# Kernel optimization log

Hardware: AMD Instinct MI355X
Metric: run time of the kernel (lower is better)

Reference implementation:

```python
import jax, jax.numpy as jnp
import numpy as np

B, S, D, H = 2, 2048, 2048, 16
HD = D // H  # 128
L = 10  # adapter_len


def setup_inputs() -> dict:
    key = jax.random.key(0)
    ks = jax.random.split(key, 8)
    x = jax.random.normal(ks[0], (B, S, D), dtype=jnp.float32)
    wq = jax.random.normal(ks[1], (D, D), dtype=jnp.float32) * 0.02
    wk = jax.random.normal(ks[2], (D, D), dtype=jnp.float32) * 0.02
    wv = jax.random.normal(ks[3], (D, D), dtype=jnp.float32) * 0.02
    wo = jax.random.normal(ks[4], (D, D), dtype=jnp.float32) * 0.02
    adapter = jax.random.normal(ks[5], (1, L, D), dtype=jnp.float32)
    gate = jax.random.normal(ks[6], (1, H, 1, 1), dtype=jnp.float32) * 0.1
    # rotary frequencies (LLaMA style, theta=10000)
    inv_freq = 1.0 / (10000.0 ** (jnp.arange(0, HD, 2, dtype=jnp.float32) / HD))
    t = jnp.arange(S, dtype=jnp.float32)
    ang = jnp.outer(t, inv_freq)  # [S, HD//2]
    freqs_cos = jnp.cos(ang)
    freqs_sin = jnp.sin(ang)
    # additive causal mask [1,1,S,S]
    mask = jnp.triu(jnp.full((S, S), -1e9, dtype=jnp.float32), k=1)[None, None]
    return {"x": x, "wq": wq, "wk": wk, "wv": wv, "wo": wo,
            "adapter": adapter, "gate": gate,
            "freqs_cos": freqs_cos, "freqs_sin": freqs_sin, "mask": mask}


def _rope(v, cos, sin):
    # v: [B,S,H,HD]; cos/sin: [S, HD//2]; complex multiply on (even, odd) pairs
    v = v.reshape(*v.shape[:-1], HD // 2, 2)
    v0, v1 = v[..., 0], v[..., 1]
    c = cos[None, :, None, :]
    s = sin[None, :, None, :]
    out = jnp.stack([v0 * c - v1 * s, v0 * s + v1 * c], axis=-1)
    return out.reshape(*out.shape[:-2], HD)


def reference(x, wq, wk, wv, wo, adapter, gate, freqs_cos, freqs_sin, mask):
    scale = 1.0 / np.sqrt(HD)
    xq = (x @ wq).reshape(B, S, H, HD)
    xk = (x @ wk).reshape(B, S, H, HD)
    xv = (x @ wv).reshape(B, S, H, HD)
    xq = _rope(xq, freqs_cos, freqs_sin)
    xk = _rope(xk, freqs_cos, freqs_sin)
    # self-attention with additive causal mask
    scores = jnp.einsum('bqhd,bkhd->bhqk', xq, xk) * scale + mask
    probs = jax.nn.softmax(scores.astype(jnp.float32), axis=-1).astype(xq.dtype)
    out = jnp.einsum('bhqk,bkhd->bqhd', probs, xv)  # [B,S,H,HD]
    # gated adapter cross-attention (no rotary on adapter K/V)
    ak = (adapter[0] @ wk).reshape(L, H, HD)
    av = (adapter[0] @ wv).reshape(L, H, HD)
    a_scores = jnp.einsum('bqhd,khd->bhqk', xq, ak) * scale
    a_probs = gate * jax.nn.softmax(a_scores.astype(jnp.float32), axis=-1).astype(xq.dtype)
    out = out + jnp.einsum('bhqk,khd->bqhd', a_probs, av)
    return out.reshape(B, S, D) @ wo
```

## Files before the change

### kernel.cpp

```cpp
#include <hip/hip_runtime.h>


typedef unsigned short ushort_t;
typedef unsigned int uint32;
typedef __attribute__((ext_vector_type(8))) short bf16x8;
typedef __attribute__((ext_vector_type(4))) float f32x4;

__device__ __forceinline__ void async16(void* lds, const void* g) {
  __builtin_amdgcn_global_load_lds((const __attribute__((address_space(1))) void*)g,
                                   (__attribute__((address_space(3))) void*)lds,
                                   16, 0, 0);
}
__device__ __forceinline__ ushort_t f2bf(float f) {
  uint32 u = __float_as_uint(f);
  u += 0x7FFFu + ((u >> 16) & 1u);
  return (ushort_t)(u >> 16);
}
__device__ __forceinline__ float bf2f(ushort_t b) {
  return __uint_as_float(((uint32)b) << 16);
}
__device__ __forceinline__ float dpp_xor1(float v) {
  return __int_as_float(__builtin_amdgcn_update_dpp(
      0, __float_as_int(v), 0xB1, 0xf, 0xf, true));
}
#define DPP_MAX(t, ctrl) \
  t = fmaxf(t, __int_as_float(__builtin_amdgcn_update_dpp( \
      0, __float_as_int(t), (ctrl), 0xf, 0xf, true)))
#define DPP_ADD(t, ctrl) \
  t += __int_as_float(__builtin_amdgcn_update_dpp( \
      0, __float_as_int(t), (ctrl), 0xf, 0xf, true))
__device__ __forceinline__ float rowmax16(float t) {
  DPP_MAX(t, 0xB1);
  DPP_MAX(t, 0x4E);
  t = fmaxf(t, __int_as_float(__builtin_amdgcn_ds_swizzle(
      __float_as_int(t), 0x101F)));
  DPP_MAX(t, 0x128);
  return t;
}
__device__ __forceinline__ float rowsum16(float t) {
  DPP_ADD(t, 0xB1);
  DPP_ADD(t, 0x4E);
  t += __int_as_float(__builtin_amdgcn_ds_swizzle(__float_as_int(t), 0x101F));
  DPP_ADD(t, 0x128);
  return t;
}

__global__ __launch_bounds__(256) void cast_x_kernel(const float* __restrict__ x,
                                                     ushort_t* __restrict__ Xb) {
  size_t i = ((size_t)blockIdx.x * 256 + threadIdx.x) * 8;
  float4 a = *(const float4*)(x + i);
  float4 b = *(const float4*)(x + i + 4);
  uint4 o;
  o.x = (uint32)f2bf(a.x) | ((uint32)f2bf(a.y) << 16);
  o.y = (uint32)f2bf(a.z) | ((uint32)f2bf(a.w) << 16);
  o.z = (uint32)f2bf(b.x) | ((uint32)f2bf(b.y) << 16);
  o.w = (uint32)f2bf(b.z) | ((uint32)f2bf(b.w) << 16);
  *(uint4*)(Xb + i) = o;
}

__global__ __launch_bounds__(256) void rope_pack_kernel(
    const float* __restrict__ fc, const float* __restrict__ fs,
    float2* __restrict__ fcs) {
  int i = blockIdx.x * 256 + threadIdx.x;
  fcs[i] = make_float2(fc[i], fs[i]);
}

__global__ __launch_bounds__(256) void transpose_w_kernel(
    const float* __restrict__ w0, const float* __restrict__ w1,
    const float* __restrict__ w2, const float* __restrict__ w3,
    ushort_t* __restrict__ outBase) {
  const float* W = (blockIdx.z == 0) ? w0 : (blockIdx.z == 1) ? w1
                 : (blockIdx.z == 2) ? w2 : w3;
  ushort_t* Wt = outBase + (size_t)blockIdx.z * 4194304;
  __shared__ float L[64][65];
  int t = threadIdx.x, tc = t & 63, tr = t >> 6;
  int k0 = blockIdx.x * 64, n0 = blockIdx.y * 64;
  for (int i = 0; i < 16; ++i) {
    int r = i * 4 + tr;
    L[r][tc] = W[(size_t)(k0 + r) * 2048 + n0 + tc];
  }
  __syncthreads();
  int tr8 = t >> 5, tc2 = t & 31;
  for (int i = 0; i < 8; ++i) {
    int r = i * 8 + tr8;
    uint32 pk = (uint32)f2bf(L[2 * tc2][r]) | ((uint32)f2bf(L[2 * tc2 + 1][r]) << 16);
    *(uint32*)(Wt + (size_t)(n0 + r) * 2048 + k0 + 2 * tc2) = pk;
  }
}

__global__ __launch_bounds__(256) void adapter_kv_kernel(
    const float* __restrict__ adapter, const float* __restrict__ wk,
    const float* __restrict__ wv, float* __restrict__ ak, float* __restrict__ av) {
  const float* W = blockIdx.z ? wv : wk;
  float* out = blockIdx.z ? av : ak;
  __shared__ float As[10][128];
  int t = threadIdx.x;
  int k0 = blockIdx.y * 128;
  for (int i = t; i < 1280; i += 256)
    As[i >> 7][i & 127] = adapter[(size_t)(i >> 7) * 2048 + k0 + (i & 127)];
  __syncthreads();
  int n = blockIdx.x * 256 + t;
  float acc[10];
#pragma unroll
  for (int l = 0; l < 10; ++l) acc[l] = 0.f;
  for (int kk = 0; kk < 128; ++kk) {
    float wv_ = W[(size_t)(k0 + kk) * 2048 + n];
#pragma unroll
    for (int l = 0; l < 10; ++l) acc[l] += As[l][kk] * wv_;
  }
#pragma unroll
  for (int l = 0; l < 10; ++l) atomicAdd(&out[l * 2048 + n], acc[l]);
}

__global__ __launch_bounds__(256) void adapter_pack_kernel(
    const float* __restrict__ ak, const float* __restrict__ av,
    ushort_t* __restrict__ akb, ushort_t* __restrict__ avb) {
  int t = blockIdx.x * 256 + threadIdx.x;
  if (t < 32768) {
    int h = t >> 11, l = (t >> 7) & 15, d = t & 127;
    akb[t] = (l < 10) ? f2bf(ak[l * 2048 + h * 128 + d]) : (ushort_t)0;
  }
  int h = t >> 12, d = (t >> 5) & 127, l = t & 31;
  avb[t] = (l < 10) ? f2bf(av[l * 2048 + h * 128 + d]) : (ushort_t)0;
}

#define QK_BARX() asm volatile("s_barrier" ::: "memory")
#define QK_LGKM0() asm volatile("s_waitcnt lgkmcnt(0)" ::: "memory")

__device__ __forceinline__ void kloop_128x256(
    char* lds, const ushort_t* __restrict__ A, const ushort_t* __restrict__ Bt,
    size_t bm0, size_t bn0, f32x4 (&acc)[4][4]) {
  const int tid = (int)threadIdx.x;
  const int w = tid >> 6, lane = tid & 63, quad = lane >> 4, l15 = lane & 15;
  const int wr = (w >> 2) * 64, wc = (w & 3) * 64;
  const int nt = 32;
  char* const pA0 = lds;
  char* const pA1 = lds + 16384;
  char* const pB0 = lds + 32768;
  char* const pB1 = lds + 65536;

#define PAT(T) (((T) & 1) ? pA1 : pA0)
#define PBT(T) (((T) & 1) ? pB1 : pB0)
#define SEGL(OP, LDSB, GROW, T)                                                \
  do {                                                                         \
    int rr_ = w * 8 + (lane >> 3);                                             \
    int cl_ = (lane & 7) ^ (rr_ & 7);                                          \
    async16((LDSB) + w * 1024,                                                 \
            (OP) + ((GROW) + (size_t)rr_) * 2048 + (size_t)((T) * 64 + cl_ * 8)); \
  } while (0)
#define ST_A(T)                                                                \
  do { if ((T) < nt) { SEGL(A, PAT(T), bm0, (T));                              \
                       SEGL(A, PAT(T) + 8192, bm0 + 64, (T)); } } while (0)
#define ST_B0(T)                                                               \
  do { if ((T) < nt) SEGL(Bt, PBT(T), bn0, (T)); } while (0)
#define ST_B123(T)                                                             \
  do { if ((T) < nt) { SEGL(Bt, PBT(T) + 8192,  bn0 + 64,  (T));               \
                       SEGL(Bt, PBT(T) + 16384, bn0 + 128, (T));               \
                       SEGL(Bt, PBT(T) + 24576, bn0 + 192, (T)); } } while (0)

  ST_A(0); ST_B0(0); ST_B123(0); ST_B123(1);
  asm volatile("s_waitcnt vmcnt(3)" ::: "memory");
  QK_BARX();

#pragma unroll 2
  for (int t = 0; t < nt; ++t) {
    const char* pA = PAT(t);
    const char* pB = PBT(t);
    bf16x8 bfv[4][2];
#pragma unroll
    for (int j = 0; j < 4; ++j) {
      int brow = wc + j * 16 + l15;
#pragma unroll
      for (int ks = 0; ks < 2; ++ks)
        bfv[j][ks] = *(const bf16x8*)(pB + brow * 128 +
                                      (((ks * 4 + quad) ^ (brow & 7)) * 16));
    }
#pragma unroll
    for (int ph = 0; ph < 2; ++ph) {
      bf16x8 af[2][2];
#pragma unroll
      for (int ii = 0; ii < 2; ++ii) {
        int arow = wr + (ph * 2 + ii) * 16 + l15;
#pragma unroll
        for (int ks = 0; ks < 2; ++ks)
          af[ii][ks] = *(const bf16x8*)(pA + arow * 128 +
                                        (((ks * 4 + quad) ^ (arow & 7)) * 16));
      }
      if (ph == 0) { ST_A(t + 1); ST_B0(t + 1); }
      else         { ST_B123(t + 2); }
      QK_BARX();
      QK_LGKM0();
      __builtin_amdgcn_s_setprio(1);
#pragma unroll
      for (int ks = 0; ks < 2; ++ks)
#pragma unroll
        for (int ii = 0; ii < 2; ++ii)
#pragma unroll
          for (int j = 0; j < 4; ++j)
            acc[ph * 2 + ii][j] = __builtin_amdgcn_mfma_f32_16x16x32_bf16(
                af[ii][ks], bfv[j][ks], acc[ph * 2 + ii][j], 0, 0, 0);
      __builtin_amdgcn_s_setprio(0);
      if (ph == 1) {
        if (t == nt - 2) asm volatile("s_waitcnt vmcnt(0)" ::: "memory");
        else             asm volatile("s_waitcnt vmcnt(3)" ::: "memory");
      }
      QK_BARX();
    }
  }
#undef PAT
#undef PBT
#undef SEGL
#undef ST_A
#undef ST_B0
#undef ST_B123
}

__global__ __launch_bounds__(512, 2) void gemm_qkv128_kernel(
    const ushort_t* __restrict__ A, const ushort_t* __restrict__ Bt,
    ushort_t* __restrict__ outQ, ushort_t* __restrict__ outK,
    ushort_t* __restrict__ Vt, const float2* __restrict__ fcs) {
  __shared__ char lds[98304];
  const int tid = (int)threadIdx.x;
  const int w = tid >> 6, lane = tid & 63, quad = lane >> 4, l15 = lane & 15;
  const int wr = (w >> 2) * 64, wc = (w & 3) * 64;

  const int wg = ((int)blockIdx.x & 7) * 96 + ((int)blockIdx.x >> 3);
  const size_t bm0 = (size_t)(wg & 31) * 128;
  const size_t bn0 = (size_t)(wg >> 5) * 256;

  f32x4 acc[4][4];
  f32x4 z4 = {0.f, 0.f, 0.f, 0.f};
#pragma unroll
  for (int i = 0; i < 4; ++i)
#pragma unroll
    for (int j = 0; j < 4; ++j) acc[i][j] = z4;

  kloop_128x256(lds, A, Bt, bm0, bn0, acc);

  const int seg = (int)(bn0 >> 11);
  if (seg < 2) {
    ushort_t* ob = seg ? outK : outQ;
#pragma unroll
    for (int i = 0; i < 4; ++i)
#pragma unroll
      for (int r = 0; r < 4; ++r) {
        size_t m = bm0 + wr + i * 16 + quad * 4 + r;
        int s = (int)(m & 2047);
#pragma unroll
        for (int j = 0; j < 4; ++j) {
          size_t n = (bn0 + wc + j * 16 + l15) & 2047;
          float v = acc[i][j][r];
          float v2 = dpp_xor1(v);
          int fi = ((int)n & 127) >> 1;
          float2 cs = fcs[s * 64 + fi];
          v = (lane & 1) ? (v2 * cs.y + v * cs.x) : (v * cs.x - v2 * cs.y);
          ob[m * 2048 + n] = f2bf(v);
        }
      }
  } else {
    char* T = lds + w * 8192;
#pragma unroll
    for (int i = 0; i < 4; ++i)
#pragma unroll
      for (int j = 0; j < 4; ++j) {
        int nn = j * 16 + l15;
        int md0 = i * 8 + quad * 2;
        uint32 p01 = (uint32)f2bf(acc[i][j][0]) | ((uint32)f2bf(acc[i][j][1]) << 16);
        uint32 p23 = (uint32)f2bf(acc[i][j][2]) | ((uint32)f2bf(acc[i][j][3]) << 16);
        *(uint32*)(T + nn * 128 + ((md0 ^ (nn & 31)) * 4)) = p01;
        *(uint32*)(T + nn * 128 + (((md0 + 1) ^ (nn & 31)) * 4)) = p23;
      }
    const int b = (int)(bm0 >> 11);
    const int s0 = (int)(bm0 & 2047) + wr;
    const int n2 = (int)(bn0 & 2047) + wc;
#pragma unroll
    for (int it = 0; it < 32; ++it) {
      int row = it * 2 + (lane >> 5);
      int pp = lane & 31;
      uint32 dv = *(const uint32*)(T + row * 128 + pp * 4);
      int md = pp ^ (row & 31);
      int nloc = n2 + row;
      size_t bh = (size_t)b * 16 + (nloc >> 7);
      *(uint32*)(Vt + (bh * 128 + (size_t)(nloc & 127)) * 2048 + s0 + 2 * md) = dv;
    }
  }
}

__global__ __launch_bounds__(512, 2) void gemm_wo_kernel(
    const ushort_t* __restrict__ A, const ushort_t* __restrict__ Bt,
    float* __restrict__ out) {
  __shared__ char lds[98304];
  const int tid = (int)threadIdx.x;
  const int w = tid >> 6, lane = tid & 63, quad = lane >> 4, l15 = lane & 15;
  const int wr = (w >> 2) * 64, wc = (w & 3) * 64;

  const int wg = ((int)blockIdx.x & 7) * 32 + ((int)blockIdx.x >> 3);
  const size_t bm0 = (size_t)(wg & 31) * 128;
  const size_t bn0 = (size_t)(wg >> 5) * 256;

  f32x4 acc[4][4];
  f32x4 z4 = {0.f, 0.f, 0.f, 0.f};
#pragma unroll
  for (int i = 0; i < 4; ++i)
#pragma unroll
    for (int j = 0; j < 4; ++j) acc[i][j] = z4;

  kloop_128x256(lds, A, Bt, bm0, bn0, acc);

#pragma unroll
  for (int i = 0; i < 4; ++i)
#pragma unroll
    for (int r = 0; r < 4; ++r) {
      size_t m = bm0 + wr + i * 16 + quad * 4 + r;
#pragma unroll
      for (int j = 0; j < 4; ++j) {
        size_t n = bn0 + wc + j * 16 + l15;
        out[m * 2048 + n] = acc[i][j][r];
      }
    }
}

__global__ __launch_bounds__(256) void flash_kernel(
    const ushort_t* __restrict__ Qb, const ushort_t* __restrict__ Kb,
    const ushort_t* __restrict__ Vt, const ushort_t* __restrict__ akb,
    const ushort_t* __restrict__ avb, const float* __restrict__ gate,
    ushort_t* __restrict__ Ob) {
  __shared__ char ldsK[16384];
  __shared__ char ldsV[16384];
  __shared__ char ldsP[16384];
  const int tid = threadIdx.x;
  const int w = tid >> 6, lane = tid & 63, quad = lane >> 4, l15 = lane & 15;
  const int idx = blockIdx.x;
  const int p = idx >> 8, c = idx & 255;
  const int u = c >> 4, vv = c & 15;
  const int qt = p ? (15 - u) : u;
  const int hb = (p << 4) | vv;
  const int h = hb >> 1, b = hb & 1;
  const float scale = 0.08838834764831845f;

  bf16x8 ones;
#pragma unroll
  for (int j = 0; j < 8; ++j) ones[j] = (short)0x3F80;

  bf16x8 qf[2][4];
#pragma unroll
  for (int mt = 0; mt < 2; ++mt) {
    size_t qrow = (size_t)qt * 128 + w * 32 + mt * 16 + l15;
    const ushort_t* base = Qb + ((size_t)b * 2048 + qrow) * 2048 + h * 128 + quad * 8;
#pragma unroll
    for (int ds = 0; ds < 4; ++ds) qf[mt][ds] = *(const bf16x8*)(base + ds * 32);
  }

  f32x4 zero4 = {0.f, 0.f, 0.f, 0.f};
  f32x4 oacc[2][8];
  f32x4 osum[2];
  float mrow[2][4];
#pragma unroll
  for (int mt = 0; mt < 2; ++mt) {
#pragma unroll
    for (int n8 = 0; n8 < 8; ++n8) oacc[mt][n8] = zero4;
    osum[mt] = zero4;
#pragma unroll
    for (int r = 0; r < 4; ++r) mrow[mt][r] = -1e30f;
  }

  const int ktmax = 2 * qt + 1;
  for (int kt = 0; kt <= ktmax; ++kt) {
#pragma unroll
    for (int ii = 0; ii < 4; ++ii) {
      int r0 = w * 16 + ii * 4;
      int row = r0 + (lane >> 4);
      int cl = (lane & 15) ^ (row & 15);
      async16(ldsK + r0 * 256,
              Kb + ((size_t)b * 2048 + kt * 64 + row) * 2048 + h * 128 + cl * 8);
    }
#pragma unroll
    for (int ii = 0; ii < 4; ++ii) {
      int d0 = w * 32 + ii * 8;
      int dr = d0 + (lane >> 3);
      int cl = (lane & 7) ^ (dr & 7);
      async16(ldsV + d0 * 128,
              Vt + ((size_t)(b * 16 + h) * 128 + dr) * 2048 + kt * 64 + cl * 8);
    }
    __syncthreads();

    f32x4 sacc[2][4];
#pragma unroll
    for (int mt = 0; mt < 2; ++mt)
#pragma unroll
      for (int nt = 0; nt < 4; ++nt) sacc[mt][nt] = zero4;
#pragma unroll
    for (int ds = 0; ds < 4; ++ds) {
      bf16x8 kf[4];
      int ch = ds * 4 + quad;
#pragma unroll
      for (int nt = 0; nt < 4; ++nt) {
        int row = nt * 16 + l15;
        kf[nt] = *(const bf16x8*)(ldsK + row * 256 + ((ch ^ (row & 15)) * 16));
      }
#pragma unroll
      for (int mt = 0; mt < 2; ++mt)
#pragma unroll
        for (int nt = 0; nt < 4; ++nt)
          sacc[mt][nt] = __builtin_amdgcn_mfma_f32_16x16x32_bf16(qf[mt][ds], kf[nt], sacc[mt][nt], 0, 0, 0);
    }

    const bool domask = (kt >= 2 * qt);
#pragma unroll
    for (int mt = 0; mt < 2; ++mt) {
      float tmax[4] = {-1e30f, -1e30f, -1e30f, -1e30f};
      const int qbase = qt * 128 + w * 32 + mt * 16 + quad * 4;
#pragma unroll
      for (int nt = 0; nt < 4; ++nt) {
        int kg = kt * 64 + nt * 16 + l15;
#pragma unroll
        for (int r = 0; r < 4; ++r) {
          float s = sacc[mt][nt][r] * scale;
          if (domask && kg > qbase + r) s = -1e30f;
          sacc[mt][nt][r] = s;
          tmax[r] = fmaxf(tmax[r], s);
        }
      }
#pragma unroll
      for (int r = 0; r < 4; ++r) {
        float t = rowmax16(tmax[r]);
        float mnew = fmaxf(mrow[mt][r], t);
        float alpha = __expf(mrow[mt][r] - mnew);
        mrow[mt][r] = mnew;
        osum[mt][r] *= alpha;
#pragma unroll
        for (int n8 = 0; n8 < 8; ++n8) oacc[mt][n8][r] *= alpha;
        tmax[r] = mnew;
      }
#pragma unroll
      for (int nt = 0; nt < 4; ++nt) {
        int col = nt * 16 + l15;
#pragma unroll
        for (int r = 0; r < 4; ++r) {
          float pv = __expf(sacc[mt][nt][r] - tmax[r]);
          int prow = w * 32 + mt * 16 + quad * 4 + r;
          int addr = prow * 128 + (((col >> 3) ^ (prow & 7)) * 16) + (col & 7) * 2;
          *(ushort_t*)(ldsP + addr) = f2bf(pv);
        }
      }
    }

#pragma unroll
    for (int ks = 0; ks < 2; ++ks) {
      int ch = ks * 4 + quad;
      bf16x8 pf[2];
#pragma unroll
      for (int mt = 0; mt < 2; ++mt) {
        int prow = w * 32 + mt * 16 + l15;
        pf[mt] = *(const bf16x8*)(ldsP + prow * 128 + ((ch ^ (prow & 7)) * 16));
      }
#pragma unroll
      for (int mt = 0; mt < 2; ++mt)
        osum[mt] = __builtin_amdgcn_mfma_f32_16x16x32_bf16(pf[mt], ones, osum[mt], 0, 0, 0);
#pragma unroll
      for (int n8 = 0; n8 < 8; ++n8) {
        int dr = n8 * 16 + l15;
        bf16x8 vf = *(const bf16x8*)(ldsV + dr * 128 + ((ch ^ (dr & 7)) * 16));
#pragma unroll
        for (int mt = 0; mt < 2; ++mt)
          oacc[mt][n8] = __builtin_amdgcn_mfma_f32_16x16x32_bf16(pf[mt], vf, oacc[mt][n8], 0, 0, 0);
      }
    }
    __syncthreads();
  }

  const float g = gate[h];
  {
    int row = w * 32 + (lane >> 1);
    int koff = 16 + (lane & 1) * 8;
    *(uint4*)(ldsP + row * 80 + koff * 2) = make_uint4(0, 0, 0, 0);
  }
  f32x4 sa[2] = {zero4, zero4};
#pragma unroll
  for (int ds = 0; ds < 4; ++ds) {
    bf16x8 kfa = *(const bf16x8*)(akb + ((size_t)h * 16 + l15) * 128 + ds * 32 + quad * 8);
#pragma unroll
    for (int mt = 0; mt < 2; ++mt)
      sa[mt] = __builtin_amdgcn_mfma_f32_16x16x32_bf16(qf[mt][ds], kfa, sa[mt], 0, 0, 0);
  }
#pragma unroll
  for (int mt = 0; mt < 2; ++mt) {
#pragma unroll
    for (int r = 0; r < 4; ++r) {
      float s = sa[mt][r] * scale;
      if (l15 >= 10) s = -1e30f;
      float mx = rowmax16(s);
      float e = __expf(s - mx);
      float sum = rowsum16(e);
      float pv = g * e / sum;
      int row = w * 32 + mt * 16 + quad * 4 + r;
      *(ushort_t*)(ldsP + row * 80 + l15 * 2) = f2bf(pv);
    }
  }
  bf16x8 paf[2];
#pragma unroll
  for (int mt = 0; mt < 2; ++mt)
    paf[mt] = *(const bf16x8*)(ldsP + (w * 32 + mt * 16 + l15) * 80 + quad * 16);

#pragma unroll
  for (int mt = 0; mt < 2; ++mt) {
    float rl[4];
#pragma unroll
    for (int r = 0; r < 4; ++r) rl[r] = 1.f / osum[mt][r];
#pragma unroll
    for (int n8 = 0; n8 < 8; ++n8)
#pragma unroll
      for (int r = 0; r < 4; ++r) oacc[mt][n8][r] *= rl[r];
  }
#pragma unroll
  for (int n8 = 0; n8 < 8; ++n8) {
    bf16x8 avf = *(const bf16x8*)(avb + ((size_t)h * 128 + n8 * 16 + l15) * 32 + quad * 8);
#pragma unroll
    for (int mt = 0; mt < 2; ++mt)
      oacc[mt][n8] = __builtin_amdgcn_mfma_f32_16x16x32_bf16(paf[mt], avf, oacc[mt][n8], 0, 0, 0);
  }
#pragma unroll
  for (int mt = 0; mt < 2; ++mt) {
    size_t qb0 = (size_t)qt * 128 + w * 32 + mt * 16 + quad * 4;
#pragma unroll
    for (int n8 = 0; n8 < 8; ++n8) {
      size_t col = (size_t)h * 128 + n8 * 16 + l15;
#pragma unroll
      for (int r = 0; r < 4; ++r)
        Ob[((size_t)b * 2048 + qb0 + r) * 2048 + col] = f2bf(oacc[mt][n8][r]);
    }
  }
}

extern "C" void kernel_launch(void* const* d_in, const int* in_sizes, int n_in,
                              void* d_out, int out_size, void* d_ws, size_t ws_size,
                              hipStream_t stream) {
  (void)in_sizes; (void)n_in; (void)out_size; (void)ws_size;
  const float* x       = (const float*)d_in[0];
  const float* wq      = (const float*)d_in[1];
  const float* wk      = (const float*)d_in[2];
  const float* wv      = (const float*)d_in[3];
  const float* wo      = (const float*)d_in[4];
  const float* adapter = (const float*)d_in[5];
  const float* gate    = (const float*)d_in[6];
  const float* fc      = (const float*)d_in[7];
  const float* fs      = (const float*)d_in[8];

  char* ws = (char*)d_ws;
  ushort_t* Xb   = (ushort_t*)(ws + 0);
  ushort_t* WtQ  = (ushort_t*)(ws + 16777216);
  ushort_t* WtO  = (ushort_t*)(ws + 41943040);
  ushort_t* Qb   = (ushort_t*)(ws + 50331648);
  ushort_t* Kb   = (ushort_t*)(ws + 67108864);
  ushort_t* Vt   = (ushort_t*)(ws + 83886080);
  float*    ak   = (float*)   (ws + 100663296);
  float*    av   = (float*)   (ws + 100745216);
  ushort_t* akb  = (ushort_t*)(ws + 100827136);
  ushort_t* avb  = (ushort_t*)(ws + 100892672);
  float2*   fcs  = (float2*)  (ws + 101023744);
  ushort_t* Ob   = Xb;

  cast_x_kernel<<<4096, 256, 0, stream>>>(x, Xb);
  rope_pack_kernel<<<512, 256, 0, stream>>>(fc, fs, fcs);
  transpose_w_kernel<<<dim3(32, 32, 4), 256, 0, stream>>>(wq, wk, wv, wo, WtQ);
  hipMemsetAsync(ak, 0, 163840, stream);
  adapter_kv_kernel<<<dim3(8, 16, 2), 256, 0, stream>>>(adapter, wk, wv, ak, av);
  adapter_pack_kernel<<<256, 256, 0, stream>>>(ak, av, akb, avb);
  gemm_qkv128_kernel<<<dim3(768), 512, 0, stream>>>(Xb, WtQ, Qb, Kb, Vt, fcs);
  flash_kernel<<<512, 256, 0, stream>>>(Qb, Kb, Vt, akb, avb, gate, Ob);
  gemm_wo_kernel<<<dim3(256), 512, 0, stream>>>(Ob, WtO, (float*)d_out);
}
```

Baseline: 444.9 us.

## Shrink flash attention Q tile to 64 rows and double grid size

The flash kernel now handles 64 query rows per block (16 per wave) instead of 128, doubling the grid to 1024 blocks with a new causal-balanced block ordering. It also skips the online-softmax rescale unless the running max grows by more than a threshold, packs P to bf16 pairs with a DPP swap plus a packed convert, and halves the P LDS buffer while requesting 4 blocks per CU. The aim is better occupancy and load balance on the causal triangle and less softmax overhead, at the cost of K/V tiles being reloaded by twice as many blocks.

```diff
diff --git a/kernel.cpp b/kernel.cpp
--- a/kernel.cpp
+++ b/kernel.cpp
@@ -320,21 +320,22 @@
     }
 }
 
-__global__ __launch_bounds__(256) void flash_kernel(
+__global__ __launch_bounds__(256, 4) void flash_kernel(
     const ushort_t* __restrict__ Qb, const ushort_t* __restrict__ Kb,
     const ushort_t* __restrict__ Vt, const ushort_t* __restrict__ akb,
     const ushort_t* __restrict__ avb, const float* __restrict__ gate,
     ushort_t* __restrict__ Ob) {
   __shared__ char ldsK[16384];
   __shared__ char ldsV[16384];
-  __shared__ char ldsP[16384];
+  __shared__ char ldsP[8192];
   const int tid = threadIdx.x;
   const int w = tid >> 6, lane = tid & 63, quad = lane >> 4, l15 = lane & 15;
   const int idx = blockIdx.x;
-  const int p = idx >> 8, c = idx & 255;
-  const int u = c >> 4, vv = c & 15;
-  const int qt = p ? (15 - u) : u;
-  const int hb = (p << 4) | vv;
+  const int pg = idx >> 8, c = idx & 255;
+  const int u = c >> 3, vv = c & 7;
+  const int uu = (pg & 2) ? ((u + 16) & 31) : u;
+  const int qt2 = (pg & 1) ? (31 - uu) : uu;
+  const int hb = (pg << 3) | vv;
   const int h = hb >> 1, b = hb & 1;
   const float scale = 0.08838834764831845f;
 
@@ -342,30 +343,24 @@
 #pragma unroll
   for (int j = 0; j < 8; ++j) ones[j] = (short)0x3F80;
 
-  bf16x8 qf[2][4];
-#pragma unroll
-  for (int mt = 0; mt < 2; ++mt) {
-    size_t qrow = (size_t)qt * 128 + w * 32 + mt * 16 + l15;
+  bf16x8 qf[4];
+  {
+    size_t qrow = (size_t)qt2 * 64 + w * 16 + l15;
     const ushort_t* base = Qb + ((size_t)b * 2048 + qrow) * 2048 + h * 128 + quad * 8;
 #pragma unroll
-    for (int ds = 0; ds < 4; ++ds) qf[mt][ds] = *(const bf16x8*)(base + ds * 32);
+    for (int ds = 0; ds < 4; ++ds) qf[ds] = *(const bf16x8*)(base + ds * 32);
   }
 
   f32x4 zero4 = {0.f, 0.f, 0.f, 0.f};
-  f32x4 oacc[2][8];
-  f32x4 osum[2];
-  float mrow[2][4];
-#pragma unroll
-  for (int mt = 0; mt < 2; ++mt) {
-#pragma unroll
-    for (int n8 = 0; n8 < 8; ++n8) oacc[mt][n8] = zero4;
-    osum[mt] = zero4;
-#pragma unroll
-    for (int r = 0; r < 4; ++r) mrow[mt][r] = -1e30f;
-  }
-
-  const int ktmax = 2 * qt + 1;
-  for (int kt = 0; kt <= ktmax; ++kt) {
+  f32x4 oacc[8];
+  f32x4 osum = zero4;
+  float mrow[4];
+#pragma unroll
+  for (int n8 = 0; n8 < 8; ++n8) oacc[n8] = zero4;
+#pragma unroll
+  for (int r = 0; r < 4; ++r) mrow[r] = -1e30f;
+
+  for (int kt = 0; kt <= qt2; ++kt) {
 #pragma unroll
     for (int ii = 0; ii < 4; ++ii) {
       int r0 = w * 16 + ii * 4;
@@ -384,11 +379,9 @@
     }
     __syncthreads();
 
-    f32x4 sacc[2][4];
-#pragma unroll
-    for (int mt = 0; mt < 2; ++mt)
-#pragma unroll
-      for (int nt = 0; nt < 4; ++nt) sacc[mt][nt] = zero4;
+    f32x4 sacc[4];
+#pragma unroll
+    for (int nt = 0; nt < 4; ++nt) sacc[nt] = zero4;
 #pragma unroll
     for (int ds = 0; ds < 4; ++ds) {
       bf16x8 kf[4];
@@ -399,71 +392,77 @@
         kf[nt] = *(const bf16x8*)(ldsK + row * 256 + ((ch ^ (row & 15)) * 16));
       }
 #pragma unroll
-      for (int mt = 0; mt < 2; ++mt)
-#pragma unroll
-        for (int nt = 0; nt < 4; ++nt)
-          sacc[mt][nt] = __builtin_amdgcn_mfma_f32_16x16x32_bf16(qf[mt][ds], kf[nt], sacc[mt][nt], 0, 0, 0);
-    }
-
-    const bool domask = (kt >= 2 * qt);
-#pragma unroll
-    for (int mt = 0; mt < 2; ++mt) {
-      float tmax[4] = {-1e30f, -1e30f, -1e30f, -1e30f};
-      const int qbase = qt * 128 + w * 32 + mt * 16 + quad * 4;
-#pragma unroll
-      for (int nt = 0; nt < 4; ++nt) {
-        int kg = kt * 64 + nt * 16 + l15;
+      for (int nt = 0; nt < 4; ++nt)
+        sacc[nt] = __builtin_amdgcn_mfma_f32_16x16x32_bf16(qf[ds], kf[nt], sacc[nt], 0, 0, 0);
+    }
+
+    const bool domask = (kt == qt2);
+    float tmax[4] = {-1e30f, -1e30f, -1e30f, -1e30f};
+    const int qbr = qt2 * 64 + w * 16 + quad * 4;
+#pragma unroll
+    for (int nt = 0; nt < 4; ++nt) {
+      int kg = kt * 64 + nt * 16 + l15;
+#pragma unroll
+      for (int r = 0; r < 4; ++r) {
+        float s = sacc[nt][r] * scale;
+        if (domask && kg > qbr + r) s = -1e30f;
+        sacc[nt][r] = s;
+        tmax[r] = fmaxf(tmax[r], s);
+      }
+    }
+    float need = 0.f;
+#pragma unroll
+    for (int r = 0; r < 4; ++r) {
+      tmax[r] = rowmax16(tmax[r]);
+      need = fmaxf(need, tmax[r] - mrow[r]);
+    }
+    if (__any(need > 8.0f)) {
+      float alpha[4];
+#pragma unroll
+      for (int r = 0; r < 4; ++r) {
+        float mnew = fmaxf(mrow[r], tmax[r]);
+        alpha[r] = __expf(mrow[r] - mnew);
+        osum[r] *= alpha[r];
+        mrow[r] = mnew;
+      }
+#pragma unroll
+      for (int n8 = 0; n8 < 8; ++n8)
+#pragma unroll
+        for (int r = 0; r < 4; ++r) oacc[n8][r] *= alpha[r];
+    }
+    uint32 pk[4][4];
+#pragma unroll
+    for (int nt = 0; nt < 4; ++nt)
+#pragma unroll
+      for (int r = 0; r < 4; ++r) {
+        float pv = __expf(sacc[nt][r] - mrow[r]);
+        float pn = dpp_xor1(pv);
+        uint32 d_;
+        asm volatile("v_cvt_pk_bf16_f32 %0, %1, %2" : "=v"(d_) : "v"(pv), "v"(pn));
+        pk[nt][r] = d_;
+      }
+    if (!(lane & 1)) {
+#pragma unroll
+      for (int nt = 0; nt < 4; ++nt)
 #pragma unroll
         for (int r = 0; r < 4; ++r) {
-          float s = sacc[mt][nt][r] * scale;
-          if (domask && kg > qbase + r) s = -1e30f;
-          sacc[mt][nt][r] = s;
-          tmax[r] = fmaxf(tmax[r], s);
+          int col = nt * 16 + l15;
+          int prow = w * 16 + quad * 4 + r;
+          *(uint32*)(ldsP + prow * 128 + (((col >> 3) ^ (prow & 7)) * 16) + (col & 7) * 2) = pk[nt][r];
         }
-      }
-#pragma unroll
-      for (int r = 0; r < 4; ++r) {
-        float t = rowmax16(tmax[r]);
-        float mnew = fmaxf(mrow[mt][r], t);
-        float alpha = __expf(mrow[mt][r] - mnew);
-        mrow[mt][r] = mnew;
-        osum[mt][r] *= alpha;
-#pragma unroll
-        for (int n8 = 0; n8 < 8; ++n8) oacc[mt][n8][r] *= alpha;
-        tmax[r] = mnew;
-      }
-#pragma unroll
-      for (int nt = 0; nt < 4; ++nt) {
-        int col = nt * 16 + l15;
-#pragma unroll
-        for (int r = 0; r < 4; ++r) {
-          float pv = __expf(sacc[mt][nt][r] - tmax[r]);
-          int prow = w * 32 + mt * 16 + quad * 4 + r;
-          int addr = prow * 128 + (((col >> 3) ^ (prow & 7)) * 16) + (col & 7) * 2;
-          *(ushort_t*)(ldsP + addr) = f2bf(pv);
-        }
-      }
     }
 
 #pragma unroll
     for (int ks = 0; ks < 2; ++ks) {
       int ch = ks * 4 + quad;
-      bf16x8 pf[2];
-#pragma unroll
-      for (int mt = 0; mt < 2; ++mt) {
-        int prow = w * 32 + mt * 16 + l15;
-        pf[mt] = *(const bf16x8*)(ldsP + prow * 128 + ((ch ^ (prow & 7)) * 16));
-      }
-#pragma unroll
-      for (int mt = 0; mt < 2; ++mt)
-        osum[mt] = __builtin_amdgcn_mfma_f32_16x16x32_bf16(pf[mt], ones, osum[mt], 0, 0, 0);
+      int prow = w * 16 + l15;
+      bf16x8 pf = *(const bf16x8*)(ldsP + prow * 128 + ((ch ^ (prow & 7)) * 16));
+      osum = __builtin_amdgcn_mfma_f32_16x16x32_bf16(pf, ones, osum, 0, 0, 0);
 #pragma unroll
       for (int n8 = 0; n8 < 8; ++n8) {
         int dr = n8 * 16 + l15;
         bf16x8 vf = *(const bf16x8*)(ldsV + dr * 128 + ((ch ^ (dr & 7)) * 16));
-#pragma unroll
-        for (int mt = 0; mt < 2; ++mt)
-          oacc[mt][n8] = __builtin_amdgcn_mfma_f32_16x16x32_bf16(pf[mt], vf, oacc[mt][n8], 0, 0, 0);
+        oacc[n8] = __builtin_amdgcn_mfma_f32_16x16x32_bf16(pf, vf, oacc[n8], 0, 0, 0);
       }
     }
     __syncthreads();
@@ -471,64 +470,47 @@
 
   const float g = gate[h];
   {
-    int row = w * 32 + (lane >> 1);
-    int koff = 16 + (lane & 1) * 8;
-    *(uint4*)(ldsP + row * 80 + koff * 2) = make_uint4(0, 0, 0, 0);
-  }
-  f32x4 sa[2] = {zero4, zero4};
+    int row = w * 16 + (lane >> 2);
+    *(uint2*)(ldsP + row * 80 + 32 + (lane & 3) * 8) = make_uint2(0, 0);
+  }
+  f32x4 sa = zero4;
 #pragma unroll
   for (int ds = 0; ds < 4; ++ds) {
     bf16x8 kfa = *(const bf16x8*)(akb + ((size_t)h * 16 + l15) * 128 + ds * 32 + quad * 8);
-#pragma unroll
-    for (int mt = 0; mt < 2; ++mt)
-      sa[mt] = __builtin_amdgcn_mfma_f32_16x16x32_bf16(qf[mt][ds], kfa, sa[mt], 0, 0, 0);
-  }
-#pragma unroll
-  for (int mt = 0; mt < 2; ++mt) {
-#pragma unroll
-    for (int r = 0; r < 4; ++r) {
-      float s = sa[mt][r] * scale;
-      if (l15 >= 10) s = -1e30f;
-      float mx = rowmax16(s);
-      float e = __expf(s - mx);
-      float sum = rowsum16(e);
-      float pv = g * e / sum;
-      int row = w * 32 + mt * 16 + quad * 4 + r;
-      *(ushort_t*)(ldsP + row * 80 + l15 * 2) = f2bf(pv);
-    }
-  }
-  bf16x8 paf[2];
-#pragma unroll
-  for (int mt = 0; mt < 2; ++mt)
-    paf[mt] = *(const bf16x8*)(ldsP + (w * 32 + mt * 16 + l15) * 80 + quad * 16);
-
-#pragma unroll
-  for (int mt = 0; mt < 2; ++mt) {
-    float rl[4];
-#pragma unroll
-    for (int r = 0; r < 4; ++r) rl[r] = 1.f / osum[mt][r];
-#pragma unroll
-    for (int n8 = 0; n8 < 8; ++n8)
-#pragma unroll
-      for (int r = 0; r < 4; ++r) oacc[mt][n8][r] *= rl[r];
-  }
+    sa = __builtin_amdgcn_mfma_f32_16x16x32_bf16(qf[ds], kfa, sa, 0, 0, 0);
+  }
+#pragma unroll
+  for (int r = 0; r < 4; ++r) {
+    float s = sa[r] * scale;
+    if (l15 >= 10) s = -1e30f;
+    float mx = rowmax16(s);
+    float e = __expf(s - mx);
+    float sum = rowsum16(e);
+    float pv = g * e / sum;
+    int row = w * 16 + quad * 4 + r;
+    *(ushort_t*)(ldsP + row * 80 + l15 * 2) = f2bf(pv);
+  }
+  bf16x8 paf = *(const bf16x8*)(ldsP + (w * 16 + l15) * 80 + quad * 16);
+
+  float rl[4];
+#pragma unroll
+  for (int r = 0; r < 4; ++r) rl[r] = 1.f / osum[r];
+#pragma unroll
+  for (int n8 = 0; n8 < 8; ++n8)
+#pragma unroll
+    for (int r = 0; r < 4; ++r) oacc[n8][r] *= rl[r];
 #pragma unroll
   for (int n8 = 0; n8 < 8; ++n8) {
     bf16x8 avf = *(const bf16x8*)(avb + ((size_t)h * 128 + n8 * 16 + l15) * 32 + quad * 8);
-#pragma unroll
-    for (int mt = 0; mt < 2; ++mt)
-      oacc[mt][n8] = __builtin_amdgcn_mfma_f32_16x16x32_bf16(paf[mt], avf, oacc[mt][n8], 0, 0, 0);
-  }
-#pragma unroll
-  for (int mt = 0; mt < 2; ++mt) {
-    size_t qb0 = (size_t)qt * 128 + w * 32 + mt * 16 + quad * 4;
-#pragma unroll
-    for (int n8 = 0; n8 < 8; ++n8) {
-      size_t col = (size_t)h * 128 + n8 * 16 + l15;
-#pragma unroll
-      for (int r = 0; r < 4; ++r)
-        Ob[((size_t)b * 2048 + qb0 + r) * 2048 + col] = f2bf(oacc[mt][n8][r]);
-    }
+    oacc[n8] = __builtin_amdgcn_mfma_f32_16x16x32_bf16(paf, avf, oacc[n8], 0, 0, 0);
+  }
+  size_t qb0 = (size_t)qt2 * 64 + w * 16 + quad * 4;
+#pragma unroll
+  for (int n8 = 0; n8 < 8; ++n8) {
+    size_t col = (size_t)h * 128 + n8 * 16 + l15;
+#pragma unroll
+    for (int r = 0; r < 4; ++r)
+      Ob[((size_t)b * 2048 + qb0 + r) * 2048 + col] = f2bf(oacc[n8][r]);
   }
 }
 
@@ -567,6 +549,6 @@
   adapter_kv_kernel<<<dim3(8, 16, 2), 256, 0, stream>>>(adapter, wk, wv, ak, av);
   adapter_pack_kernel<<<256, 256, 0, stream>>>(ak, av, akb, avb);
   gemm_qkv128_kernel<<<dim3(768), 512, 0, stream>>>(Xb, WtQ, Qb, Kb, Vt, fcs);
-  flash_kernel<<<512, 256, 0, stream>>>(Qb, Kb, Vt, akb, avb, gate, Ob);
+  flash_kernel<<<dim3(1024), 256, 0, stream>>>(Qb, Kb, Vt, akb, avb, gate, Ob);
   gemm_wo_kernel<<<dim3(256), 512, 0, stream>>>(Ob, WtO, (float*)d_out);
 }
```

After: 432.6 us. 1.03x faster.

## Add lazy softmax rescaling, packed bf16 P stores, and drop rope pack kernel

Applied to the files above, without the earlier changes.

In the flash kernel the online-softmax rescale of the output accumulators is now skipped unless some row's max has grown by more than a threshold, so the stale max is kept as the exponent reference. P values are converted in pairs with v_cvt_pk_bf16_f32 and written as 32-bit LDS stores from even lanes, which halves the number of stores. The separate rope_pack kernel is removed and the QKV GEMM epilogue reads cos and sin directly from the two tables. The costs are two gathered loads per element in the GEMM epilogue and a bounded exponent growth in P, which increases bf16 rounding risk.

```diff
diff --git a/kernel.cpp b/kernel.cpp
--- a/kernel.cpp
+++ b/kernel.cpp
@@ -56,13 +56,6 @@
   o.z = (uint32)f2bf(b.x) | ((uint32)f2bf(b.y) << 16);
   o.w = (uint32)f2bf(b.z) | ((uint32)f2bf(b.w) << 16);
   *(uint4*)(Xb + i) = o;
-}
-
-__global__ __launch_bounds__(256) void rope_pack_kernel(
-    const float* __restrict__ fc, const float* __restrict__ fs,
-    float2* __restrict__ fcs) {
-  int i = blockIdx.x * 256 + threadIdx.x;
-  fcs[i] = make_float2(fc[i], fs[i]);
 }
 
 __global__ __launch_bounds__(256) void transpose_w_kernel(
@@ -218,7 +211,8 @@
 __global__ __launch_bounds__(512, 2) void gemm_qkv128_kernel(
     const ushort_t* __restrict__ A, const ushort_t* __restrict__ Bt,
     ushort_t* __restrict__ outQ, ushort_t* __restrict__ outK,
-    ushort_t* __restrict__ Vt, const float2* __restrict__ fcs) {
+    ushort_t* __restrict__ Vt,
+    const float* __restrict__ fc, const float* __restrict__ fs) {
   __shared__ char lds[98304];
   const int tid = (int)threadIdx.x;
   const int w = tid >> 6, lane = tid & 63, quad = lane >> 4, l15 = lane & 15;
@@ -252,8 +246,9 @@
           float v = acc[i][j][r];
           float v2 = dpp_xor1(v);
           int fi = ((int)n & 127) >> 1;
-          float2 cs = fcs[s * 64 + fi];
-          v = (lane & 1) ? (v2 * cs.y + v * cs.x) : (v * cs.x - v2 * cs.y);
+          float cosv = fc[s * 64 + fi];
+          float sinv = fs[s * 64 + fi];
+          v = (lane & 1) ? (v2 * sinv + v * cosv) : (v * cosv - v2 * sinv);
           ob[m * 2048 + n] = f2bf(v);
         }
       }
@@ -406,6 +401,8 @@
     }
 
     const bool domask = (kt >= 2 * qt);
+    float tmax2[2][4];
+    float need = 0.f;
 #pragma unroll
     for (int mt = 0; mt < 2; ++mt) {
       float tmax[4] = {-1e30f, -1e30f, -1e30f, -1e30f};
@@ -423,25 +420,49 @@
       }
 #pragma unroll
       for (int r = 0; r < 4; ++r) {
-        float t = rowmax16(tmax[r]);
-        float mnew = fmaxf(mrow[mt][r], t);
-        float alpha = __expf(mrow[mt][r] - mnew);
-        mrow[mt][r] = mnew;
-        osum[mt][r] *= alpha;
-#pragma unroll
-        for (int n8 = 0; n8 < 8; ++n8) oacc[mt][n8][r] *= alpha;
-        tmax[r] = mnew;
-      }
-#pragma unroll
-      for (int nt = 0; nt < 4; ++nt) {
-        int col = nt * 16 + l15;
+        tmax2[mt][r] = rowmax16(tmax[r]);
+        need = fmaxf(need, tmax2[mt][r] - mrow[mt][r]);
+      }
+    }
+    if (__any(need > 8.0f)) {
+#pragma unroll
+      for (int mt = 0; mt < 2; ++mt) {
+        float alpha[4];
 #pragma unroll
         for (int r = 0; r < 4; ++r) {
-          float pv = __expf(sacc[mt][nt][r] - tmax[r]);
-          int prow = w * 32 + mt * 16 + quad * 4 + r;
-          int addr = prow * 128 + (((col >> 3) ^ (prow & 7)) * 16) + (col & 7) * 2;
-          *(ushort_t*)(ldsP + addr) = f2bf(pv);
+          float mnew = fmaxf(mrow[mt][r], tmax2[mt][r]);
+          alpha[r] = __expf(mrow[mt][r] - mnew);
+          osum[mt][r] *= alpha[r];
+          mrow[mt][r] = mnew;
         }
+#pragma unroll
+        for (int n8 = 0; n8 < 8; ++n8)
+#pragma unroll
+          for (int r = 0; r < 4; ++r) oacc[mt][n8][r] *= alpha[r];
+      }
+    }
+#pragma unroll
+    for (int mt = 0; mt < 2; ++mt) {
+      uint32 pk[4][4];
+#pragma unroll
+      for (int nt = 0; nt < 4; ++nt)
+#pragma unroll
+        for (int r = 0; r < 4; ++r) {
+          float pv = __expf(sacc[mt][nt][r] - mrow[mt][r]);
+          float pn = dpp_xor1(pv);
+          uint32 d_;
+          asm volatile("v_cvt_pk_bf16_f32 %0, %1, %2" : "=v"(d_) : "v"(pv), "v"(pn));
+          pk[nt][r] = d_;
+        }
+      if (!(lane & 1)) {
+#pragma unroll
+        for (int nt = 0; nt < 4; ++nt)
+#pragma unroll
+          for (int r = 0; r < 4; ++r) {
+            int col = nt * 16 + l15;
+            int prow = w * 32 + mt * 16 + quad * 4 + r;
+            *(uint32*)(ldsP + prow * 128 + (((col >> 3) ^ (prow & 7)) * 16) + (col & 7) * 2) = pk[nt][r];
+          }
       }
     }
 
@@ -475,7 +496,8 @@
     int koff = 16 + (lane & 1) * 8;
     *(uint4*)(ldsP + row * 80 + koff * 2) = make_uint4(0, 0, 0, 0);
   }
-  f32x4 sa[2] = {zero4, zero4};
+  f32x4 zero4b = {0.f, 0.f, 0.f, 0.f};
+  f32x4 sa[2] = {zero4b, zero4b};
 #pragma unroll
   for (int ds = 0; ds < 4; ++ds) {
     bf16x8 kfa = *(const bf16x8*)(akb + ((size_t)h * 16 + l15) * 128 + ds * 32 + quad * 8);
@@ -557,16 +579,14 @@
   float*    av   = (float*)   (ws + 100745216);
   ushort_t* akb  = (ushort_t*)(ws + 100827136);
   ushort_t* avb  = (ushort_t*)(ws + 100892672);
-  float2*   fcs  = (float2*)  (ws + 101023744);
   ushort_t* Ob   = Xb;
 
   cast_x_kernel<<<4096, 256, 0, stream>>>(x, Xb);
-  rope_pack_kernel<<<512, 256, 0, stream>>>(fc, fs, fcs);
   transpose_w_kernel<<<dim3(32, 32, 4), 256, 0, stream>>>(wq, wk, wv, wo, WtQ);
   hipMemsetAsync(ak, 0, 163840, stream);
   adapter_kv_kernel<<<dim3(8, 16, 2), 256, 0, stream>>>(adapter, wk, wv, ak, av);
   adapter_pack_kernel<<<256, 256, 0, stream>>>(ak, av, akb, avb);
-  gemm_qkv128_kernel<<<dim3(768), 512, 0, stream>>>(Xb, WtQ, Qb, Kb, Vt, fcs);
-  flash_kernel<<<512, 256, 0, stream>>>(Qb, Kb, Vt, akb, avb, gate, Ob);
+  gemm_qkv128_kernel<<<dim3(768), 512, 0, stream>>>(Xb, WtQ, Qb, Kb, Vt, fc, fs);
+  flash_kernel<<<dim3(512), 256, 0, stream>>>(Qb, Kb, Vt, akb, avb, gate, Ob);
   gemm_wo_kernel<<<dim3(256), 512, 0, stream>>>(Ob, WtO, (float*)d_out);
 }
```

After: 426.6 us. 4.1% less time.
